# Performance work log

Measured on AMD Instinct MI355X. Metric: run time of the kernel, lower is better.

The kernel has to match this reference:

```python
import jax, jax.numpy as jnp
import numpy as np

N = 4096
F_IN = 256
HEADS = 8
FEAT = 64
NEG_SLOPE = 0.2


def setup_inputs() -> dict:
    key = jax.random.key(0)
    k_x, k_adj, k_w, k_s, k_d = jax.random.split(key, 5)
    x = jax.random.normal(k_x, (N, F_IN), dtype=jnp.float32)
    adj = (jax.random.uniform(k_adj, (N, N)) < 0.02).astype(jnp.float32)
    W = jax.random.normal(k_w, (F_IN, HEADS * FEAT), dtype=jnp.float32) * (1.0 / np.sqrt(F_IN))
    a_src = jax.random.normal(k_s, (FEAT,), dtype=jnp.float32) * (1.0 / np.sqrt(FEAT))
    a_dst = jax.random.normal(k_d, (FEAT,), dtype=jnp.float32) * (1.0 / np.sqrt(FEAT))
    return {"x": x, "adj": adj, "W": W, "a_src": a_src, "a_dst": a_dst}


def reference(x, adj, W, a_src, a_dst):
    n = x.shape[0]
    adj = adj + jnp.eye(n, dtype=adj.dtype)          # add self loops
    h = (x @ W).reshape(n, HEADS, FEAT)              # (N, H, F)
    s_src = jnp.einsum('nhf,f->nh', h, a_src)        # (N, H)
    s_dst = jnp.einsum('nhf,f->nh', h, a_dst)        # (N, H)
    # e[i, j, h] = leaky_relu(s_src[i,h] + s_dst[j,h])  -> (N, N, H)
    e = jax.nn.leaky_relu(s_src[:, None, :] + s_dst[None, :, :], negative_slope=NEG_SLOPE)
    mask = (adj == 0)                                # (N, N)
    e = jnp.where(mask[:, :, None], -1e9, e)
    alpha = jax.nn.softmax(e, axis=1)                # softmax over neighbor axis j
    out = jnp.einsum('ijh,jhf->ihf', alpha, h)       # (N, H, F)
    return out.reshape(n, HEADS * FEAT)              # concat heads -> (N, 512)
```

## Files before the change

### kernel.cpp

```cpp
#include <hip/hip_runtime.h>
#include <hip/hip_fp16.h>
#include <stdint.h>

#define NROWS 4096
#define FIN   256
#define NHEADS 8
#define HF    512
#define NEG   0.2f
#define MAXDEG 144

typedef _Float16 half8_t  __attribute__((ext_vector_type(8)));
typedef float    float4_t __attribute__((ext_vector_type(4)));
typedef float    f4v      __attribute__((ext_vector_type(4)));

__global__ __launch_bounds__(256) void k_stage(const float* __restrict__ adj,
                                               const float* __restrict__ x,
                                               const float* __restrict__ W,
                                               uint16_t* __restrict__ nbr_g,
                                               int* __restrict__ deg,
                                               _Float16* __restrict__ xh,
                                               _Float16* __restrict__ Wt) {
    __shared__ uint16_t cnbr[4][MAXDEG];
    const int bid = blockIdx.x, t = threadIdx.x;

    if (bid < 1024) {
        const int w = t >> 6, lane = t & 63;
        const int row = bid*4 + w;

        uint32_t* nb32 = (uint32_t*)cnbr[w];
        nb32[lane] = 0;
        if (lane < (MAXDEG/2 - 64)) nb32[64 + lane] = 0;
        __builtin_amdgcn_wave_barrier();

        const f4v* ar = (const f4v*)(adj + (size_t)row * NROWS + lane*4);
        f4v f[16];
        #pragma unroll
        for (int k = 0; k < 16; ++k) f[k] = __builtin_nontemporal_load(ar + k*64);

        uint64_t pm = 0;
        #pragma unroll
        for (int k = 0; k < 16; ++k) {
            if (f[k].x != 0.f) pm |= 1ull << (k*4+0);
            if (f[k].y != 0.f) pm |= 1ull << (k*4+1);
            if (f[k].z != 0.f) pm |= 1ull << (k*4+2);
            if (f[k].w != 0.f) pm |= 1ull << (k*4+3);
        }
        if (((row >> 2) & 63) == lane)
            pm |= 1ull << (((row >> 8) << 2) | (row & 3));

        int pcnt = __popcll(pm);
        int incl = pcnt;
        #pragma unroll
        for (int d = 1; d < 64; d <<= 1) {
            int u = __shfl_up(incl, d);
            if (lane >= d) incl += u;
        }
        int cnt = __shfl(incl, 63);
        int pos = incl - pcnt;
        if (cnt > MAXDEG) cnt = MAXDEG;

        uint64_t m = pm;
        while (m) {
            int q = (int)__ffsll((unsigned long long)m) - 1;  m &= m - 1;
            int col = ((q >> 2) << 8) + lane*4 + (q & 3);
            if (pos < MAXDEG) cnbr[w][pos] = (uint16_t)col;
            pos++;
        }
        __builtin_amdgcn_wave_barrier();

        uint32_t* og = (uint32_t*)(nbr_g + (size_t)row * MAXDEG);
        og[lane] = nb32[lane];
        if (lane < (MAXDEG/2 - 64)) og[64 + lane] = nb32[64 + lane];
        if (lane == 0) deg[row] = cnt;
    } else if (bid < 2048) {
        const int i4 = ((bid - 1024)*256 + t) * 4;
        f4v v = __builtin_nontemporal_load((const f4v*)&x[i4]);
        union { _Float16 h[4]; uint2 u; } P;
        P.h[0] = (_Float16)v.x; P.h[1] = (_Float16)v.y;
        P.h[2] = (_Float16)v.z; P.h[3] = (_Float16)v.w;
        *(uint2*)&xh[i4] = P.u;
    } else {
        const int i4 = ((bid - 2048)*256 + t) * 4;
        const int n = i4 >> 8, k0 = i4 & 255;
        union { _Float16 h[4]; uint2 u; } P;
        P.h[0] = (_Float16)W[(size_t)(k0+0)*HF + n];
        P.h[1] = (_Float16)W[(size_t)(k0+1)*HF + n];
        P.h[2] = (_Float16)W[(size_t)(k0+2)*HF + n];
        P.h[3] = (_Float16)W[(size_t)(k0+3)*HF + n];
        *(uint2*)&Wt[(size_t)n*FIN + k0] = P.u;
    }
}

__global__ __launch_bounds__(256) void k_gemm(const _Float16* __restrict__ xh,
                                              const _Float16* __restrict__ Wt,
                                              const float* __restrict__ a_src,
                                              const float* __restrict__ a_dst,
                                              _Float16* __restrict__ hfp,
                                              float* __restrict__ s_src,
                                              float* __restrict__ s_dst) {
    __shared__ _Float16 Ah[64][72];
    __shared__ _Float16 Bh[64][72];
    const int t = threadIdx.x;
    const int bm = blockIdx.x >> 3, bn = blockIdx.x & 7;
    const int lane = t & 63, w = t >> 6;
    const int wm = (w & 1) * 32, wn = (w >> 1) * 32;
    const int mrow = lane & 15, kch = (lane >> 4) * 8;
    const int sr = t >> 2, sc = (t & 3) << 4;

    float4_t acc00{}, acc01{}, acc10{}, acc11{};

    for (int kt = 0; kt < FIN; kt += 64) {
        uint4 a0 = *(const uint4*)&xh[(size_t)(bm*64 + sr)*FIN + kt + sc];
        uint4 a1 = *(const uint4*)&xh[(size_t)(bm*64 + sr)*FIN + kt + sc + 8];
        uint4 b0 = *(const uint4*)&Wt[(size_t)(bn*64 + sr)*FIN + kt + sc];
        uint4 b1 = *(const uint4*)&Wt[(size_t)(bn*64 + sr)*FIN + kt + sc + 8];
        __syncthreads();
        *(uint4*)&Ah[sr][sc]     = a0;  *(uint4*)&Ah[sr][sc + 8] = a1;
        *(uint4*)&Bh[sr][sc]     = b0;  *(uint4*)&Bh[sr][sc + 8] = b1;
        __syncthreads();
        #pragma unroll
        for (int kk = 0; kk < 64; kk += 32) {
            half8_t fa0 = *(const half8_t*)&Ah[wm + mrow][kk + kch];
            half8_t fa1 = *(const half8_t*)&Ah[wm + 16 + mrow][kk + kch];
            half8_t fb0 = *(const half8_t*)&Bh[wn + mrow][kk + kch];
            half8_t fb1 = *(const half8_t*)&Bh[wn + 16 + mrow][kk + kch];
            acc00 = __builtin_amdgcn_mfma_f32_16x16x32_f16(fa0, fb0, acc00, 0, 0, 0);
            acc01 = __builtin_amdgcn_mfma_f32_16x16x32_f16(fa0, fb1, acc01, 0, 0, 0);
            acc10 = __builtin_amdgcn_mfma_f32_16x16x32_f16(fa1, fb0, acc10, 0, 0, 0);
            acc11 = __builtin_amdgcn_mfma_f32_16x16x32_f16(fa1, fb1, acc11, 0, 0, 0);
        }
    }

    __syncthreads();
    const int crow = (lane >> 4) * 4;
    #pragma unroll
    for (int r = 0; r < 4; ++r) {
        Ah[wm + crow + r][wn + mrow]           = (_Float16)acc00[r];
        Ah[wm + crow + r][wn + 16 + mrow]      = (_Float16)acc01[r];
        Ah[wm + 16 + crow + r][wn + mrow]      = (_Float16)acc10[r];
        Ah[wm + 16 + crow + r][wn + 16 + mrow] = (_Float16)acc11[r];
    }
    __syncthreads();

    uint4 h0 = *(const uint4*)&Ah[sr][sc];
    uint4 h1 = *(const uint4*)&Ah[sr][sc + 8];
    *(uint4*)&hfp[(size_t)(bm*64 + sr)*HF + bn*64 + sc]     = h0;
    *(uint4*)&hfp[(size_t)(bm*64 + sr)*HF + bn*64 + sc + 8] = h1;

    union { uint4 u[2]; _Float16 h[16]; } H; H.u[0] = h0; H.u[1] = h1;
    float ps = 0.f, pd = 0.f;
    #pragma unroll
    for (int e = 0; e < 16; ++e) {
        float hv = (float)H.h[e];
        ps += hv * a_src[sc + e];
        pd += hv * a_dst[sc + e];
    }
    ps += __shfl_xor(ps, 1); ps += __shfl_xor(ps, 2);
    pd += __shfl_xor(pd, 1); pd += __shfl_xor(pd, 2);
    if ((t & 3) == 0) {
        s_src[(bm*64 + sr)*NHEADS + bn] = ps;
        s_dst[(bm*64 + sr)*NHEADS + bn] = pd;
    }
}

__global__ __launch_bounds__(64) void k_agg(const uint16_t* __restrict__ nbr_g,
                                            const int* __restrict__ deg,
                                            const float* __restrict__ s_src,
                                            const float* __restrict__ s_dst,
                                            const _Float16* __restrict__ hfp,
                                            float* __restrict__ out) {
    __shared__ float    abuf[MAXDEG][4];
    __shared__ uint32_t nbrs[MAXDEG];

    const int lane = threadIdx.x;
    const int wid  = blockIdx.x;
    const int row  = wid >> 1, half = wid & 1;

    int cnt = deg[row];
    if (cnt > MAXDEG) cnt = MAXDEG;
    const int pad8 = (cnt + 7) & ~7;

    const uint32_t* src32 = (const uint32_t*)(nbr_g + (size_t)row * MAXDEG);
    uint32_t v0 = src32[lane];
    nbrs[2*lane]     = (v0 & 0xffffu) << 10;
    nbrs[2*lane + 1] = (v0 >> 16) << 10;
    if (lane < (MAXDEG/2 - 64)) {
        uint32_t v1 = src32[64 + lane];
        nbrs[128 + 2*lane] = (v1 & 0xffffu) << 10;
        nbrs[129 + 2*lane] = (v1 >> 16) << 10;
    }
    __builtin_amdgcn_wave_barrier();

    float4 si = *(const float4*)&s_src[row*NHEADS + half*4];
    float ac0=0, ac1=0, ac2=0, ac3=0;
    #pragma unroll 1
    for (int base = 0; base < pad8; base += 64) {
        int p = base + lane;
        if (p < pad8) {
            float a0=0, a1=0, a2=0, a3=0;
            if (p < cnt) {
                int j8 = (int)(nbrs[p] >> 10) * NHEADS;
                float4 d = *(const float4*)&s_dst[j8 + half*4];
                float e;
                e = si.x + d.x; e = e > 0.f ? e : NEG*e; a0 = __expf(e);
                e = si.y + d.y; e = e > 0.f ? e : NEG*e; a1 = __expf(e);
                e = si.z + d.z; e = e > 0.f ? e : NEG*e; a2 = __expf(e);
                e = si.w + d.w; e = e > 0.f ? e : NEG*e; a3 = __expf(e);
            }
            *(float4*)&abuf[p][0] = make_float4(a0, a1, a2, a3);
            ac0 += a0; ac1 += a1; ac2 += a2; ac3 += a3;
        }
    }
    #pragma unroll
    for (int msk = 1; msk < 64; msk <<= 1) {
        ac0 += __shfl_xor(ac0, msk); ac1 += __shfl_xor(ac1, msk);
        ac2 += __shfl_xor(ac2, msk); ac3 += __shfl_xor(ac3, msk);
    }
    const int h3 = lane >> 4;
    float tot = (h3 == 0) ? ac0 : (h3 == 1) ? ac1 : (h3 == 2) ? ac2 : ac3;
    const float invg = 1.f / tot;
    __builtin_amdgcn_wave_barrier();

    const char* hb = (const char*)hfp + half*512 + lane*8;
    float c0=0, c1=0, c2=0, c3=0;
    for (int p = 0; p < pad8; p += 8) {
        uint32_t jo[8]; uint2 hv[8]; float aa[8];
        #pragma unroll
        for (int u = 0; u < 8; ++u) jo[u] = nbrs[p + u];
        #pragma unroll
        for (int u = 0; u < 8; ++u) hv[u] = *(const uint2*)(hb + jo[u]);
        #pragma unroll
        for (int u = 0; u < 8; ++u) aa[u] = abuf[p + u][h3];
        #pragma unroll
        for (int u = 0; u < 8; ++u) {
            union { uint2 q; _Float16 h[4]; } U; U.q = hv[u];
            c0 += (float)U.h[0]*aa[u]; c1 += (float)U.h[1]*aa[u];
            c2 += (float)U.h[2]*aa[u]; c3 += (float)U.h[3]*aa[u];
        }
    }

    f4v o; o.x = c0*invg; o.y = c1*invg; o.z = c2*invg; o.w = c3*invg;
    __builtin_nontemporal_store(o, (f4v*)&out[(size_t)row*HF + half*256 + lane*4]);
}

extern "C" void kernel_launch(void* const* d_in, const int* in_sizes, int n_in,
                              void* d_out, int out_size, void* d_ws, size_t ws_size,
                              hipStream_t stream) {
    const float* x     = (const float*)d_in[0];
    const float* adj   = (const float*)d_in[1];
    const float* W     = (const float*)d_in[2];
    const float* a_src = (const float*)d_in[3];
    const float* a_dst = (const float*)d_in[4];
    float* out = (float*)d_out;

    char* ws = (char*)d_ws;
    _Float16* hfp   = (_Float16*)ws;
    float*    s_src = (float*)(ws + 4u*1024*1024);
    float*    s_dst = (float*)(ws + 4u*1024*1024 + 128u*1024);
    _Float16* xh    = (_Float16*)(ws + 4u*1024*1024 + 256u*1024);
    _Float16* Wt    = (_Float16*)(ws + 6u*1024*1024 + 256u*1024);
    uint16_t* nbr_g = (uint16_t*)(ws + 6u*1024*1024 + 512u*1024);
    int*      deg   = (int*)(ws + 7u*1024*1024 + 768u*1024);

    k_stage<<<2176, 256, 0, stream>>>(adj, x, W, nbr_g, deg, xh, Wt);
    k_gemm <<<512,  256, 0, stream>>>(xh, Wt, a_src, a_dst, hfp, s_src, s_dst);
    k_agg  <<<8192, 64,  0, stream>>>(nbr_g, deg, s_src, s_dst, hfp, out);
}
```

Baseline: 55.19 us.

## Double-buffer neighbor gathers in aggregation and pack four waves per block

The aggregation kernel now issues the gather loads for the next 8 neighbors while it consumes the current 8, using two register buffers. This aims to hide gather latency. It also packs four independent wave-rows into each 256-thread block with per-wave shared buffers, and pads neighbor counts to 16. Separately, the adjacency and x loads in the staging kernel switch from nontemporal to ordinary loads. The changes raise register pressure, and padding to 16 may add a few wasted iterations.

```diff
diff --git a/kernel.cpp b/kernel.cpp
--- a/kernel.cpp
+++ b/kernel.cpp
@@ -32,10 +32,10 @@
         if (lane < (MAXDEG/2 - 64)) nb32[64 + lane] = 0;
         __builtin_amdgcn_wave_barrier();
 
-        const f4v* ar = (const f4v*)(adj + (size_t)row * NROWS + lane*4);
-        f4v f[16];
-        #pragma unroll
-        for (int k = 0; k < 16; ++k) f[k] = __builtin_nontemporal_load(ar + k*64);
+        const float* ar = adj + (size_t)row * NROWS + lane*4;
+        float4 f[16];
+        #pragma unroll
+        for (int k = 0; k < 16; ++k) f[k] = *(const float4*)(ar + k*256);
 
         uint64_t pm = 0;
         #pragma unroll
@@ -74,7 +74,7 @@
         if (lane == 0) deg[row] = cnt;
     } else if (bid < 2048) {
         const int i4 = ((bid - 1024)*256 + t) * 4;
-        f4v v = __builtin_nontemporal_load((const f4v*)&x[i4]);
+        float4 v = *(const float4*)&x[i4];
         union { _Float16 h[4]; uint2 u; } P;
         P.h[0] = (_Float16)v.x; P.h[1] = (_Float16)v.y;
         P.h[2] = (_Float16)v.z; P.h[3] = (_Float16)v.w;
@@ -163,43 +163,43 @@
     }
 }
 
-__global__ __launch_bounds__(64) void k_agg(const uint16_t* __restrict__ nbr_g,
-                                            const int* __restrict__ deg,
-                                            const float* __restrict__ s_src,
-                                            const float* __restrict__ s_dst,
-                                            const _Float16* __restrict__ hfp,
-                                            float* __restrict__ out) {
-    __shared__ float    abuf[MAXDEG][4];
-    __shared__ uint32_t nbrs[MAXDEG];
-
-    const int lane = threadIdx.x;
-    const int wid  = blockIdx.x;
-    const int row  = wid >> 1, half = wid & 1;
+__global__ __launch_bounds__(256, 8) void k_agg(const uint16_t* __restrict__ nbr_g,
+                                                const int* __restrict__ deg,
+                                                const float* __restrict__ s_src,
+                                                const float* __restrict__ s_dst,
+                                                const _Float16* __restrict__ hfp,
+                                                float* __restrict__ out) {
+    __shared__ float    abuf[4][MAXDEG][4];
+    __shared__ uint32_t nbrs[4][MAXDEG];
+
+    const int t = threadIdx.x, w = t >> 6, lane = t & 63;
+    const int wid = blockIdx.x * 4 + w;
+    const int row = wid >> 1, half = wid & 1;
 
     int cnt = deg[row];
     if (cnt > MAXDEG) cnt = MAXDEG;
-    const int pad8 = (cnt + 7) & ~7;
+    const int pad16 = (cnt + 15) & ~15;
 
     const uint32_t* src32 = (const uint32_t*)(nbr_g + (size_t)row * MAXDEG);
     uint32_t v0 = src32[lane];
-    nbrs[2*lane]     = (v0 & 0xffffu) << 10;
-    nbrs[2*lane + 1] = (v0 >> 16) << 10;
+    nbrs[w][2*lane]     = (v0 & 0xffffu) << 10;
+    nbrs[w][2*lane + 1] = (v0 >> 16) << 10;
     if (lane < (MAXDEG/2 - 64)) {
         uint32_t v1 = src32[64 + lane];
-        nbrs[128 + 2*lane] = (v1 & 0xffffu) << 10;
-        nbrs[129 + 2*lane] = (v1 >> 16) << 10;
+        nbrs[w][128 + 2*lane] = (v1 & 0xffffu) << 10;
+        nbrs[w][129 + 2*lane] = (v1 >> 16) << 10;
     }
     __builtin_amdgcn_wave_barrier();
 
     float4 si = *(const float4*)&s_src[row*NHEADS + half*4];
     float ac0=0, ac1=0, ac2=0, ac3=0;
     #pragma unroll 1
-    for (int base = 0; base < pad8; base += 64) {
+    for (int base = 0; base < pad16; base += 64) {
         int p = base + lane;
-        if (p < pad8) {
+        if (p < pad16) {
             float a0=0, a1=0, a2=0, a3=0;
             if (p < cnt) {
-                int j8 = (int)(nbrs[p] >> 10) * NHEADS;
+                int j8 = (int)(nbrs[w][p] >> 10) * NHEADS;
                 float4 d = *(const float4*)&s_dst[j8 + half*4];
                 float e;
                 e = si.x + d.x; e = e > 0.f ? e : NEG*e; a0 = __expf(e);
@@ -207,7 +207,7 @@
                 e = si.z + d.z; e = e > 0.f ? e : NEG*e; a2 = __expf(e);
                 e = si.w + d.w; e = e > 0.f ? e : NEG*e; a3 = __expf(e);
             }
-            *(float4*)&abuf[p][0] = make_float4(a0, a1, a2, a3);
+            *(float4*)&abuf[w][p][0] = make_float4(a0, a1, a2, a3);
             ac0 += a0; ac1 += a1; ac2 += a2; ac3 += a3;
         }
     }
@@ -223,21 +223,34 @@
 
     const char* hb = (const char*)hfp + half*512 + lane*8;
     float c0=0, c1=0, c2=0, c3=0;
-    for (int p = 0; p < pad8; p += 8) {
-        uint32_t jo[8]; uint2 hv[8]; float aa[8];
-        #pragma unroll
-        for (int u = 0; u < 8; ++u) jo[u] = nbrs[p + u];
-        #pragma unroll
-        for (int u = 0; u < 8; ++u) hv[u] = *(const uint2*)(hb + jo[u]);
-        #pragma unroll
-        for (int u = 0; u < 8; ++u) aa[u] = abuf[p + u][h3];
-        #pragma unroll
-        for (int u = 0; u < 8; ++u) {
-            union { uint2 q; _Float16 h[4]; } U; U.q = hv[u];
-            c0 += (float)U.h[0]*aa[u]; c1 += (float)U.h[1]*aa[u];
-            c2 += (float)U.h[2]*aa[u]; c3 += (float)U.h[3]*aa[u];
-        }
-    }
+
+#define GISSUE(X, P)                                                        \
+    {                                                                       \
+        _Pragma("unroll") for (int u = 0; u < 8; ++u)                       \
+            hv##X[u] = *(const uint2*)(hb + nbrs[w][(P) + u]);              \
+    }
+#define GCONSUME(X, P)                                                      \
+    {                                                                       \
+        _Pragma("unroll") for (int u = 0; u < 8; ++u) {                     \
+            float av = abuf[w][(P) + u][h3];                                \
+            union { uint2 q; _Float16 h[4]; } U; U.q = hv##X[u];            \
+            c0 += (float)U.h[0]*av; c1 += (float)U.h[1]*av;                 \
+            c2 += (float)U.h[2]*av; c3 += (float)U.h[3]*av;                 \
+        }                                                                   \
+    }
+
+    uint2 hvA[8], hvB[8];
+    GISSUE(A, 0)
+    GISSUE(B, 8)
+    #pragma unroll 1
+    for (int p = 0; p < pad16; p += 16) {
+        GCONSUME(A, p)
+        if (p + 16 < pad16) GISSUE(A, p + 16)
+        GCONSUME(B, p + 8)
+        if (p + 24 < pad16) GISSUE(B, p + 24)
+    }
+#undef GISSUE
+#undef GCONSUME
 
     f4v o; o.x = c0*invg; o.y = c1*invg; o.z = c2*invg; o.w = c3*invg;
     __builtin_nontemporal_store(o, (f4v*)&out[(size_t)row*HF + half*256 + lane*4]);
@@ -264,5 +277,5 @@
 
     k_stage<<<2176, 256, 0, stream>>>(adj, x, W, nbr_g, deg, xh, Wt);
     k_gemm <<<512,  256, 0, stream>>>(xh, Wt, a_src, a_dst, hfp, s_src, s_dst);
-    k_agg  <<<8192, 64,  0, stream>>>(nbr_g, deg, s_src, s_dst, hfp, out);
-}
+    k_agg  <<<2048, 256, 0, stream>>>(nbr_g, deg, s_src, s_dst, hfp, out);
+}
```

Result: slower. 201.1 us (+264.5%).

## Fuse softmax weights into aggregation loop with one wave per row

Applied to the files above, without the earlier changes.

The aggregation kernel now handles a whole output row per wave (8 halves per lane, 4 rows per 256-thread block) instead of half a row per 64-thread block. Attention logits are computed inline per neighbor, with the softmax sum accumulated per lane, removing the separate LDS attention buffer pass and cross-lane reductions. Each lane recomputes exp for its head, so exp work is duplicated 8x across lanes in a head group. Separately, the adjacency and x loads in the staging kernel switch from nontemporal to ordinary loads.

```diff
diff --git a/kernel.cpp b/kernel.cpp
--- a/kernel.cpp
+++ b/kernel.cpp
@@ -32,10 +32,10 @@
         if (lane < (MAXDEG/2 - 64)) nb32[64 + lane] = 0;
         __builtin_amdgcn_wave_barrier();
 
-        const f4v* ar = (const f4v*)(adj + (size_t)row * NROWS + lane*4);
-        f4v f[16];
-        #pragma unroll
-        for (int k = 0; k < 16; ++k) f[k] = __builtin_nontemporal_load(ar + k*64);
+        const float* ar = adj + (size_t)row * NROWS + lane*4;
+        float4 f[16];
+        #pragma unroll
+        for (int k = 0; k < 16; ++k) f[k] = *(const float4*)(ar + k*256);
 
         uint64_t pm = 0;
         #pragma unroll
@@ -74,7 +74,7 @@
         if (lane == 0) deg[row] = cnt;
     } else if (bid < 2048) {
         const int i4 = ((bid - 1024)*256 + t) * 4;
-        f4v v = __builtin_nontemporal_load((const f4v*)&x[i4]);
+        float4 v = *(const float4*)&x[i4];
         union { _Float16 h[4]; uint2 u; } P;
         P.h[0] = (_Float16)v.x; P.h[1] = (_Float16)v.y;
         P.h[2] = (_Float16)v.z; P.h[3] = (_Float16)v.w;
@@ -163,18 +163,16 @@
     }
 }
 
-__global__ __launch_bounds__(64) void k_agg(const uint16_t* __restrict__ nbr_g,
-                                            const int* __restrict__ deg,
-                                            const float* __restrict__ s_src,
-                                            const float* __restrict__ s_dst,
-                                            const _Float16* __restrict__ hfp,
-                                            float* __restrict__ out) {
-    __shared__ float    abuf[MAXDEG][4];
-    __shared__ uint32_t nbrs[MAXDEG];
-
-    const int lane = threadIdx.x;
-    const int wid  = blockIdx.x;
-    const int row  = wid >> 1, half = wid & 1;
+__global__ __launch_bounds__(256) void k_agg(const uint16_t* __restrict__ nbr_g,
+                                             const int* __restrict__ deg,
+                                             const float* __restrict__ s_src,
+                                             const float* __restrict__ s_dst,
+                                             const _Float16* __restrict__ hfp,
+                                             float* __restrict__ out) {
+    __shared__ uint32_t nbrs[4][MAXDEG];
+
+    const int t = threadIdx.x, w = t >> 6, lane = t & 63;
+    const int row = blockIdx.x * 4 + w;
 
     int cnt = deg[row];
     if (cnt > MAXDEG) cnt = MAXDEG;
@@ -182,65 +180,52 @@
 
     const uint32_t* src32 = (const uint32_t*)(nbr_g + (size_t)row * MAXDEG);
     uint32_t v0 = src32[lane];
-    nbrs[2*lane]     = (v0 & 0xffffu) << 10;
-    nbrs[2*lane + 1] = (v0 >> 16) << 10;
+    nbrs[w][2*lane]     = v0 & 0xffffu;
+    nbrs[w][2*lane + 1] = v0 >> 16;
     if (lane < (MAXDEG/2 - 64)) {
         uint32_t v1 = src32[64 + lane];
-        nbrs[128 + 2*lane] = (v1 & 0xffffu) << 10;
-        nbrs[129 + 2*lane] = (v1 >> 16) << 10;
+        nbrs[w][128 + 2*lane] = v1 & 0xffffu;
+        nbrs[w][129 + 2*lane] = v1 >> 16;
     }
     __builtin_amdgcn_wave_barrier();
 
-    float4 si = *(const float4*)&s_src[row*NHEADS + half*4];
-    float ac0=0, ac1=0, ac2=0, ac3=0;
-    #pragma unroll 1
-    for (int base = 0; base < pad8; base += 64) {
-        int p = base + lane;
-        if (p < pad8) {
-            float a0=0, a1=0, a2=0, a3=0;
-            if (p < cnt) {
-                int j8 = (int)(nbrs[p] >> 10) * NHEADS;
-                float4 d = *(const float4*)&s_dst[j8 + half*4];
-                float e;
-                e = si.x + d.x; e = e > 0.f ? e : NEG*e; a0 = __expf(e);
-                e = si.y + d.y; e = e > 0.f ? e : NEG*e; a1 = __expf(e);
-                e = si.z + d.z; e = e > 0.f ? e : NEG*e; a2 = __expf(e);
-                e = si.w + d.w; e = e > 0.f ? e : NEG*e; a3 = __expf(e);
-            }
-            *(float4*)&abuf[p][0] = make_float4(a0, a1, a2, a3);
-            ac0 += a0; ac1 += a1; ac2 += a2; ac3 += a3;
-        }
-    }
-    #pragma unroll
-    for (int msk = 1; msk < 64; msk <<= 1) {
-        ac0 += __shfl_xor(ac0, msk); ac1 += __shfl_xor(ac1, msk);
-        ac2 += __shfl_xor(ac2, msk); ac3 += __shfl_xor(ac3, msk);
-    }
-    const int h3 = lane >> 4;
-    float tot = (h3 == 0) ? ac0 : (h3 == 1) ? ac1 : (h3 == 2) ? ac2 : ac3;
-    const float invg = 1.f / tot;
-    __builtin_amdgcn_wave_barrier();
-
-    const char* hb = (const char*)hfp + half*512 + lane*8;
-    float c0=0, c1=0, c2=0, c3=0;
+    const int h3 = lane >> 3;
+    const float si = s_src[row*NHEADS + h3];
+    const char* hb = (const char*)hfp + lane*16;
+
+    float asum = 0.f;
+    float c0=0,c1=0,c2=0,c3=0,c4=0,c5=0,c6=0,c7=0;
+
     for (int p = 0; p < pad8; p += 8) {
-        uint32_t jo[8]; uint2 hv[8]; float aa[8];
-        #pragma unroll
-        for (int u = 0; u < 8; ++u) jo[u] = nbrs[p + u];
-        #pragma unroll
-        for (int u = 0; u < 8; ++u) hv[u] = *(const uint2*)(hb + jo[u]);
-        #pragma unroll
-        for (int u = 0; u < 8; ++u) aa[u] = abuf[p + u][h3];
+        uint32_t jo[8]; float sd[8]; uint4 hv[8];
+        #pragma unroll
+        for (int u = 0; u < 8; ++u) jo[u] = nbrs[w][p + u];
+        #pragma unroll
+        for (int u = 0; u < 8; ++u) sd[u] = s_dst[jo[u]*NHEADS + h3];
+        #pragma unroll
+        for (int u = 0; u < 8; ++u)
+            hv[u] = *(const uint4*)(hb + ((size_t)jo[u] << 10));
         #pragma unroll
         for (int u = 0; u < 8; ++u) {
-            union { uint2 q; _Float16 h[4]; } U; U.q = hv[u];
-            c0 += (float)U.h[0]*aa[u]; c1 += (float)U.h[1]*aa[u];
-            c2 += (float)U.h[2]*aa[u]; c3 += (float)U.h[3]*aa[u];
-        }
-    }
-
-    f4v o; o.x = c0*invg; o.y = c1*invg; o.z = c2*invg; o.w = c3*invg;
-    __builtin_nontemporal_store(o, (f4v*)&out[(size_t)row*HF + half*256 + lane*4]);
+            float e = si + sd[u];
+            e = e > 0.f ? e : NEG * e;
+            float a = __expf(e);
+            a = (p + u < cnt) ? a : 0.f;
+            asum += a;
+            union { uint4 q; _Float16 h[8]; } U; U.q = hv[u];
+            c0 += (float)U.h[0]*a; c1 += (float)U.h[1]*a;
+            c2 += (float)U.h[2]*a; c3 += (float)U.h[3]*a;
+            c4 += (float)U.h[4]*a; c5 += (float)U.h[5]*a;
+            c6 += (float)U.h[6]*a; c7 += (float)U.h[7]*a;
+        }
+    }
+
+    const float invg = 1.f / asum;
+    float* orow = out + (size_t)row*HF + lane*8;
+    f4v o0; o0.x = c0*invg; o0.y = c1*invg; o0.z = c2*invg; o0.w = c3*invg;
+    f4v o1; o1.x = c4*invg; o1.y = c5*invg; o1.z = c6*invg; o1.w = c7*invg;
+    __builtin_nontemporal_store(o0, (f4v*)orow);
+    __builtin_nontemporal_store(o1, (f4v*)(orow + 4));
 }
 
 extern "C" void kernel_launch(void* const* d_in, const int* in_sizes, int n_in,
@@ -264,5 +249,5 @@
 
     k_stage<<<2176, 256, 0, stream>>>(adj, x, W, nbr_g, deg, xh, Wt);
     k_gemm <<<512,  256, 0, stream>>>(xh, Wt, a_src, a_dst, hfp, s_src, s_dst);
-    k_agg  <<<8192, 64,  0, stream>>>(nbr_g, deg, s_src, s_dst, hfp, out);
-}
+    k_agg  <<<1024, 256, 0, stream>>>(nbr_g, deg, s_src, s_dst, hfp, out);
+}
```

After: 49.32 us. 1.12x faster.
